# Kernel tuning notes

Hardware: AMD Instinct MI355X
Metric: run time of the kernel (lower is better)

The kernel has to match this reference:

```python
import jax, jax.numpy as jnp
import numpy as np

RADIUS = 8
EPS = 0.005

_DN = ('NCHW', 'OIHW', 'NCHW')

def _box_filter(t, r):
    """Separable normalized box filter with reflect padding. t: [H, W]."""
    ks = 2 * r + 1
    tp = jnp.pad(t, ((r, r), (r, r)), mode='reflect')[None, None]  # [1,1,H+2r,W+2r]
    kh = jnp.ones((1, 1, 1, ks), t.dtype) / ks
    kv = jnp.ones((1, 1, ks, 1), t.dtype) / ks
    out = jax.lax.conv_general_dilated(tp, kh, (1, 1), 'VALID', dimension_numbers=_DN)
    out = jax.lax.conv_general_dilated(out, kv, (1, 1), 'VALID', dimension_numbers=_DN)
    return out[0, 0]  # [H, W]

def setup_inputs() -> dict:
    key = jax.random.key(0)
    x = jax.random.uniform(key, (4096, 4096, 3), dtype=jnp.float32)
    return {"x": x}

def reference(x):
    # Rec.709 luma
    Y = 0.2126 * x[..., 0] + 0.7152 * x[..., 1] + 0.0722 * x[..., 2]  # [H,W]
    mean_I = _box_filter(Y, RADIUS)
    mean_II = _box_filter(Y * Y, RADIUS)
    var_I = mean_II - mean_I * mean_I
    a = var_I / (var_I + EPS)
    b = mean_I - a * mean_I
    mean_a = _box_filter(a, RADIUS)
    mean_b = _box_filter(b, RADIUS)
    Y_smooth = mean_a * Y + mean_b
    scale = (Y_smooth / jnp.maximum(Y, 1e-6))[..., None]  # [H,W,1]
    return jnp.clip(x * scale, 0.0, 1.0)
```

## Files before the change

kernel.cpp:

```cpp
#include <hip/hip_runtime.h>
#include <hip/hip_fp16.h>


#define HH 4096
#define WW 4096
#define RR 8
#define TILE 64
#define LD 80
#define SY_STRIDE 81
#define H_STRIDE 65
#define INV289 (1.0f / 289.0f)
#define EPSV 0.005f

__device__ __forceinline__ int reflect_idx(int i, int n) {
    i = (i < 0) ? -i : i;
    i = (i >= n) ? (2 * n - 2 - i) : i;
    return i;
}

__global__ __launch_bounds__(256) void gf_pass1(const float* __restrict__ x,
                                                __half2* __restrict__ ab) {
    __shared__ float sY[LD * SY_STRIDE];
    __shared__ float hI[LD * H_STRIDE];
    __shared__ float hII[LD * H_STRIDE];
    const int t = threadIdx.x;
    const int tx = blockIdx.x * TILE;
    const int ty = blockIdx.y * TILE;

    for (int i = t; i < LD * LD; i += 256) {
        int r = i / LD, c = i - r * LD;
        int gy = reflect_idx(ty + r - RR, HH);
        int gx = reflect_idx(tx + c - RR, WW);
        const float* p = x + (gy * WW + gx) * 3;
        sY[r * SY_STRIDE + c] = 0.2126f * p[0] + 0.7152f * p[1] + 0.0722f * p[2];
    }
    __syncthreads();

    for (int task = t; task < LD * 4; task += 256) {
        int r = task >> 2, s = task & 3;
        int base = r * SY_STRIDE + s * 16;
        int ob = r * H_STRIDE + s * 16;
        float sI = 0.f, sII = 0.f;
        #pragma unroll
        for (int k = 0; k <= 16; ++k) { float v = sY[base + k]; sI += v; sII += v * v; }
        hI[ob] = sI; hII[ob] = sII;
        #pragma unroll
        for (int j = 1; j < 16; ++j) {
            float va = sY[base + 16 + j];
            float vs = sY[base + j - 1];
            sI  += va - vs;
            sII += va * va - vs * vs;
            hI[ob + j] = sI; hII[ob + j] = sII;
        }
    }
    __syncthreads();

    const int col = t & 63;
    const int y0 = (t >> 6) * 16;
    float sI = 0.f, sII = 0.f;
    #pragma unroll
    for (int k = 0; k <= 16; ++k) {
        sI  += hI[(y0 + k) * H_STRIDE + col];
        sII += hII[(y0 + k) * H_STRIDE + col];
    }
    #pragma unroll
    for (int j = 0; j < 16; ++j) {
        float mI = sI * INV289;
        float mII = sII * INV289;
        float var = mII - mI * mI;
        float a = var / (var + EPSV);
        float b = mI - a * mI;
        ab[(ty + y0 + j) * WW + (tx + col)] = __floats2half2_rn(a, b);
        if (j < 15) {
            sI  += hI[(y0 + j + 17) * H_STRIDE + col] - hI[(y0 + j) * H_STRIDE + col];
            sII += hII[(y0 + j + 17) * H_STRIDE + col] - hII[(y0 + j) * H_STRIDE + col];
        }
    }
}

__global__ __launch_bounds__(256) void gf_pass2(const float* __restrict__ x,
                                                const __half2* __restrict__ ab,
                                                float* __restrict__ out) {
    __shared__ __half2 sAB[LD * SY_STRIDE];
    __shared__ float hA[LD * H_STRIDE];
    __shared__ float hB[LD * H_STRIDE];
    const int t = threadIdx.x;
    const int tx = blockIdx.x * TILE;
    const int ty = blockIdx.y * TILE;

    for (int i = t; i < LD * LD; i += 256) {
        int r = i / LD, c = i - r * LD;
        int gy = reflect_idx(ty + r - RR, HH);
        int gx = reflect_idx(tx + c - RR, WW);
        sAB[r * SY_STRIDE + c] = ab[gy * WW + gx];
    }
    __syncthreads();

    for (int task = t; task < LD * 4; task += 256) {
        int r = task >> 2, s = task & 3;
        int base = r * SY_STRIDE + s * 16;
        int ob = r * H_STRIDE + s * 16;
        float sA = 0.f, sB = 0.f;
        #pragma unroll
        for (int k = 0; k <= 16; ++k) {
            __half2 v = sAB[base + k];
            sA += __low2float(v); sB += __high2float(v);
        }
        hA[ob] = sA; hB[ob] = sB;
        #pragma unroll
        for (int j = 1; j < 16; ++j) {
            __half2 va = sAB[base + 16 + j];
            __half2 vs = sAB[base + j - 1];
            sA += __low2float(va)  - __low2float(vs);
            sB += __high2float(va) - __high2float(vs);
            hA[ob + j] = sA; hB[ob + j] = sB;
        }
    }
    __syncthreads();

    const int col = t & 63;
    const int y0 = (t >> 6) * 16;
    float sA = 0.f, sB = 0.f;
    #pragma unroll
    for (int k = 0; k <= 16; ++k) {
        sA += hA[(y0 + k) * H_STRIDE + col];
        sB += hB[(y0 + k) * H_STRIDE + col];
    }
    #pragma unroll
    for (int j = 0; j < 16; ++j) {
        float ma = sA * INV289;
        float mb = sB * INV289;
        int gy = ty + y0 + j, gx = tx + col;
        const float* p = x + (gy * WW + gx) * 3;
        float r0 = p[0], g0 = p[1], b0 = p[2];
        float Y = 0.2126f * r0 + 0.7152f * g0 + 0.0722f * b0;
        float scale = (ma * Y + mb) / fmaxf(Y, 1e-6f);
        float* q = out + (gy * WW + gx) * 3;
        q[0] = fminf(fmaxf(r0 * scale, 0.f), 1.f);
        q[1] = fminf(fmaxf(g0 * scale, 0.f), 1.f);
        q[2] = fminf(fmaxf(b0 * scale, 0.f), 1.f);
        if (j < 15) {
            sA += hA[(y0 + j + 17) * H_STRIDE + col] - hA[(y0 + j) * H_STRIDE + col];
            sB += hB[(y0 + j + 17) * H_STRIDE + col] - hB[(y0 + j) * H_STRIDE + col];
        }
    }
}

extern "C" void kernel_launch(void* const* d_in, const int* in_sizes, int n_in,
                              void* d_out, int out_size, void* d_ws, size_t ws_size,
                              hipStream_t stream) {
    const float* x = (const float*)d_in[0];
    float* out = (float*)d_out;
    __half2* ab = (__half2*)d_ws;
    dim3 grid(WW / TILE, HH / TILE);
    gf_pass1<<<grid, 256, 0, stream>>>(x, ab);
    gf_pass2<<<grid, 256, 0, stream>>>(x, ab, out);
}
```

Measured before the change: 432.4 us.

## Fuse both guided-filter passes into one kernel with halo recompute

Merges the two kernels into one. Each block now loads a 64x96 luma region to produce a 32x64 output tile, and keeps the a/b coefficients in shared memory instead of writing and re-reading a half2 workspace in global memory. This removes one launch and the global round trip for a/b. In exchange, overlapping halos raise redundant input reads and recomputation per output pixel. It also adds an interior fast path that skips the reflect index math.

```diff
diff --git a/kernel.cpp b/kernel.cpp
--- a/kernel.cpp
+++ b/kernel.cpp
@@ -4,11 +4,13 @@
 
 #define HH 4096
 #define WW 4096
-#define RR 8
-#define TILE 64
-#define LD 80
-#define SY_STRIDE 81
-#define H_STRIDE 65
+#define TW 32
+#define TH 64
+#define SW 64
+#define SH 96
+#define SYS 65
+#define HIS 49
+#define HAS 33
 #define INV289 (1.0f / 289.0f)
 #define EPSV 0.005f
 
@@ -18,31 +20,41 @@
     return i;
 }
 
-__global__ __launch_bounds__(256) void gf_pass1(const float* __restrict__ x,
-                                                __half2* __restrict__ ab) {
-    __shared__ float sY[LD * SY_STRIDE];
-    __shared__ float hI[LD * H_STRIDE];
-    __shared__ float hII[LD * H_STRIDE];
+__global__ __launch_bounds__(256) void gf_fused(const float* __restrict__ x,
+                                                float* __restrict__ out) {
+    __shared__ float sY[SH * SYS];
+    __shared__ float hI[SH * HIS];
+    __shared__ float hII[SH * HIS];
     const int t = threadIdx.x;
-    const int tx = blockIdx.x * TILE;
-    const int ty = blockIdx.y * TILE;
+    const int tx = blockIdx.x * TW;
+    const int ty = blockIdx.y * TH;
 
-    for (int i = t; i < LD * LD; i += 256) {
-        int r = i / LD, c = i - r * LD;
-        int gy = reflect_idx(ty + r - RR, HH);
-        int gx = reflect_idx(tx + c - RR, WW);
-        const float* p = x + (gy * WW + gx) * 3;
-        sY[r * SY_STRIDE + c] = 0.2126f * p[0] + 0.7152f * p[1] + 0.0722f * p[2];
+    const bool interior = (tx >= 16) & (tx + 48 <= WW) & (ty >= 16) & (ty + 80 <= HH);
+    if (interior) {
+        for (int idx = t; idx < SH * SW; idx += 256) {
+            int r = idx >> 6, c = idx & 63;
+            const float* p = x + (((ty + r - 16) * WW) + (tx + c - 16)) * 3;
+            sY[r * SYS + c] = 0.2126f * p[0] + 0.7152f * p[1] + 0.0722f * p[2];
+        }
+    } else {
+        for (int idx = t; idx < SH * SW; idx += 256) {
+            int r = idx >> 6, c = idx & 63;
+            int gy = reflect_idx(ty + r - 16, HH);
+            int gx = reflect_idx(tx + c - 16, WW);
+            const float* p = x + (gy * WW + gx) * 3;
+            sY[r * SYS + c] = 0.2126f * p[0] + 0.7152f * p[1] + 0.0722f * p[2];
+        }
     }
     __syncthreads();
 
-    for (int task = t; task < LD * 4; task += 256) {
-        int r = task >> 2, s = task & 3;
-        int base = r * SY_STRIDE + s * 16;
-        int ob = r * H_STRIDE + s * 16;
+    for (int task = t; task < SH * 3; task += 256) {
+        int r = task % SH;
+        int s = task / SH;
+        int base = r * SYS + s * 16;
+        int ob = r * HIS + s * 16;
         float sI = 0.f, sII = 0.f;
         #pragma unroll
-        for (int k = 0; k <= 16; ++k) { float v = sY[base + k]; sI += v; sII += v * v; }
+        for (int k = 0; k <= 16; ++k) { float w = sY[base + k]; sI += w; sII += w * w; }
         hI[ob] = sI; hII[ob] = sII;
         #pragma unroll
         for (int j = 1; j < 16; ++j) {
@@ -55,93 +67,87 @@
     }
     __syncthreads();
 
-    const int col = t & 63;
-    const int y0 = (t >> 6) * 16;
-    float sI = 0.f, sII = 0.f;
-    #pragma unroll
-    for (int k = 0; k <= 16; ++k) {
-        sI  += hI[(y0 + k) * H_STRIDE + col];
-        sII += hII[(y0 + k) * H_STRIDE + col];
-    }
-    #pragma unroll
-    for (int j = 0; j < 16; ++j) {
-        float mI = sI * INV289;
-        float mII = sII * INV289;
-        float var = mII - mI * mI;
-        float a = var / (var + EPSV);
-        float b = mI - a * mI;
-        ab[(ty + y0 + j) * WW + (tx + col)] = __floats2half2_rn(a, b);
-        if (j < 15) {
-            sI  += hI[(y0 + j + 17) * H_STRIDE + col] - hI[(y0 + j) * H_STRIDE + col];
-            sII += hII[(y0 + j + 17) * H_STRIDE + col] - hII[(y0 + j) * H_STRIDE + col];
+    __half2* ab = (__half2*)sY;
+    if (t < 240) {
+        int c = t % 48;
+        int q = t / 48;
+        int r0 = q * 16;
+        float sI = 0.f, sII = 0.f;
+        #pragma unroll
+        for (int k = 0; k <= 16; ++k) {
+            sI  += hI[(r0 + k) * HIS + c];
+            sII += hII[(r0 + k) * HIS + c];
         }
-    }
-}
-
-__global__ __launch_bounds__(256) void gf_pass2(const float* __restrict__ x,
-                                                const __half2* __restrict__ ab,
-                                                float* __restrict__ out) {
-    __shared__ __half2 sAB[LD * SY_STRIDE];
-    __shared__ float hA[LD * H_STRIDE];
-    __shared__ float hB[LD * H_STRIDE];
-    const int t = threadIdx.x;
-    const int tx = blockIdx.x * TILE;
-    const int ty = blockIdx.y * TILE;
-
-    for (int i = t; i < LD * LD; i += 256) {
-        int r = i / LD, c = i - r * LD;
-        int gy = reflect_idx(ty + r - RR, HH);
-        int gx = reflect_idx(tx + c - RR, WW);
-        sAB[r * SY_STRIDE + c] = ab[gy * WW + gx];
+        #pragma unroll
+        for (int j = 0; j < 16; ++j) {
+            int o = r0 + j;
+            float mI = sI * INV289;
+            float mII = sII * INV289;
+            float var = mII - mI * mI;
+            float a = var / (var + EPSV);
+            float b = mI - a * mI;
+            ab[o * HIS + c] = __floats2half2_rn(a, b);
+            if (j < 15) {
+                sI  += hI[(o + 17) * HIS + c] - hI[o * HIS + c];
+                sII += hII[(o + 17) * HIS + c] - hII[o * HIS + c];
+            }
+        }
     }
     __syncthreads();
 
-    for (int task = t; task < LD * 4; task += 256) {
-        int r = task >> 2, s = task & 3;
-        int base = r * SY_STRIDE + s * 16;
-        int ob = r * H_STRIDE + s * 16;
+    float* hA = hI;
+    float* hB = hII;
+    if (t < 160) {
+        int r = t % 80;
+        int s = t / 80;
+        int base = r * HIS + s * 16;
+        int ob = r * HAS + s * 16;
         float sA = 0.f, sB = 0.f;
         #pragma unroll
         for (int k = 0; k <= 16; ++k) {
-            __half2 v = sAB[base + k];
-            sA += __low2float(v); sB += __high2float(v);
+            float2 v = __half22float2(ab[base + k]);
+            sA += v.x; sB += v.y;
         }
         hA[ob] = sA; hB[ob] = sB;
         #pragma unroll
         for (int j = 1; j < 16; ++j) {
-            __half2 va = sAB[base + 16 + j];
-            __half2 vs = sAB[base + j - 1];
-            sA += __low2float(va)  - __low2float(vs);
-            sB += __high2float(va) - __high2float(vs);
+            float2 va = __half22float2(ab[base + 16 + j]);
+            float2 vs = __half22float2(ab[base + j - 1]);
+            sA += va.x - vs.x;
+            sB += va.y - vs.y;
             hA[ob + j] = sA; hB[ob + j] = sB;
         }
     }
     __syncthreads();
 
-    const int col = t & 63;
-    const int y0 = (t >> 6) * 16;
-    float sA = 0.f, sB = 0.f;
-    #pragma unroll
-    for (int k = 0; k <= 16; ++k) {
-        sA += hA[(y0 + k) * H_STRIDE + col];
-        sB += hB[(y0 + k) * H_STRIDE + col];
-    }
-    #pragma unroll
-    for (int j = 0; j < 16; ++j) {
-        float ma = sA * INV289;
-        float mb = sB * INV289;
-        int gy = ty + y0 + j, gx = tx + col;
-        const float* p = x + (gy * WW + gx) * 3;
-        float r0 = p[0], g0 = p[1], b0 = p[2];
-        float Y = 0.2126f * r0 + 0.7152f * g0 + 0.0722f * b0;
-        float scale = (ma * Y + mb) / fmaxf(Y, 1e-6f);
-        float* q = out + (gy * WW + gx) * 3;
-        q[0] = fminf(fmaxf(r0 * scale, 0.f), 1.f);
-        q[1] = fminf(fmaxf(g0 * scale, 0.f), 1.f);
-        q[2] = fminf(fmaxf(b0 * scale, 0.f), 1.f);
-        if (j < 15) {
-            sA += hA[(y0 + j + 17) * H_STRIDE + col] - hA[(y0 + j) * H_STRIDE + col];
-            sB += hB[(y0 + j + 17) * H_STRIDE + col] - hB[(y0 + j) * H_STRIDE + col];
+    {
+        int c = t & 31;
+        int q = t >> 5;
+        int r0 = q * 8;
+        float sA = 0.f, sB = 0.f;
+        #pragma unroll
+        for (int k = 0; k <= 16; ++k) {
+            sA += hA[(r0 + k) * HAS + c];
+            sB += hB[(r0 + k) * HAS + c];
+        }
+        #pragma unroll
+        for (int j = 0; j < 8; ++j) {
+            int o = r0 + j;
+            float ma = sA * INV289;
+            float mb = sB * INV289;
+            int gy = ty + o, gx = tx + c;
+            const float* p = x + (gy * WW + gx) * 3;
+            float rr = p[0], gg = p[1], bb = p[2];
+            float Y = 0.2126f * rr + 0.7152f * gg + 0.0722f * bb;
+            float scale = (ma * Y + mb) / fmaxf(Y, 1e-6f);
+            float* qo = out + (gy * WW + gx) * 3;
+            qo[0] = fminf(fmaxf(rr * scale, 0.f), 1.f);
+            qo[1] = fminf(fmaxf(gg * scale, 0.f), 1.f);
+            qo[2] = fminf(fmaxf(bb * scale, 0.f), 1.f);
+            if (j < 7) {
+                sA += hA[(o + 17) * HAS + c] - hA[o * HAS + c];
+                sB += hB[(o + 17) * HAS + c] - hB[o * HAS + c];
+            }
         }
     }
 }
@@ -151,8 +157,6 @@
                               hipStream_t stream) {
     const float* x = (const float*)d_in[0];
     float* out = (float*)d_out;
-    __half2* ab = (__half2*)d_ws;
-    dim3 grid(WW / TILE, HH / TILE);
-    gf_pass1<<<grid, 256, 0, stream>>>(x, ab);
-    gf_pass2<<<grid, 256, 0, stream>>>(x, ab, out);
+    dim3 grid(WW / TW, HH / TH);
+    gf_fused<<<grid, 256, 0, stream>>>(x, out);
 }
```

Result: faster. 400.7 us (-7.3%).
